# Kernel tuning notes

Measured on AMD Instinct MI355X. Metric: run time of the kernel, lower is better.

The kernel has to match this reference:

```python
import jax, jax.numpy as jnp
import numpy as np

H = 128; F = 64; G = 50; L = 4; CUT = 10.0
M = 256; K = 8; A = 32
N_TOPO = M * A; N = M * K * A; NCONF = M * K
E_CONF = N * 16; E_GRAPH = N_TOPO * 4
ATOM_TYPES = 100; BOND_TYPES = 10
OFFSETS = jnp.linspace(0.0, CUT, G)
GCOEFF = -0.5 / (CUT / (G - 1)) ** 2  # GaussianSmearing coeff
BN_EPS = 1e-5


def batchnorm(x, g, b):
    # BatchNorm1d in training mode: batch statistics over nodes
    mu = x.mean(0)
    var = ((x - mu) ** 2).mean(0)
    return (x - mu) * jax.lax.rsqrt(var + BN_EPS) * g + b


def setup_inputs():
    key = jax.random.key(0)
    ks = jax.random.split(key, 20)
    s = lambda k, shp: (jax.random.normal(k, shp) * 0.05).astype(jnp.float32)
    inp = {}
    inp["x_topo"] = jax.random.randint(ks[0], (N_TOPO,), 0, ATOM_TYPES)
    inp["pos"] = jax.random.normal(ks[1], (N, 3), dtype=jnp.float32) * 3.0
    inp["edge_index_conf"] = jax.random.randint(ks[2], (2, E_CONF), 0, N)
    inp["edge_index_graph"] = jax.random.randint(ks[3], (2, E_GRAPH), 0, N_TOPO)
    inp["edge_attr_graph"] = jax.random.randint(ks[4], (E_GRAPH,), 0, BOND_TYPES)
    # conf_node_batch: for molecule i, repeat arange(A)+i*A over K conformers
    cnb = (np.arange(M)[:, None, None] * A + np.broadcast_to(np.arange(A), (K, A))).reshape(-1)
    inp["conf_node_batch"] = jnp.asarray(cnb, dtype=jnp.int32)
    inp["pos_batch"] = jnp.repeat(jnp.arange(NCONF), A).astype(jnp.int32)
    inp["conf_batch"] = jnp.repeat(jnp.arange(M), K).astype(jnp.int32)
    # parameters
    inp["atom_emb"] = s(ks[5], (ATOM_TYPES, H))
    inp["cf_lin1_w"] = s(ks[6], (L, H, F))
    inp["cf_mlp_w1"] = s(ks[7], (L, G, F)); inp["cf_mlp_b1"] = jnp.zeros((L, F), jnp.float32)
    inp["cf_mlp_w2"] = s(ks[8], (L, F, F)); inp["cf_mlp_b2"] = jnp.zeros((L, F), jnp.float32)
    inp["cf_lin2_w"] = s(ks[9], (L, F, H)); inp["cf_lin2_b"] = jnp.zeros((L, H), jnp.float32)
    inp["lin_w"] = s(ks[10], (L, H, H)); inp["lin_b"] = jnp.zeros((L, H), jnp.float32)
    inp["bond_emb"] = s(ks[11], (L, BOND_TYPES, H))
    inp["gin_w1"] = s(ks[12], (L, H, H)); inp["gin_b1"] = jnp.zeros((L, H), jnp.float32)
    inp["gin_w2"] = s(ks[13], (L, H, H)); inp["gin_b2"] = jnp.zeros((L, H), jnp.float32)
    inp["gin_bn_g"] = jnp.ones((L, H), jnp.float32); inp["gin_bn_b"] = jnp.zeros((L, H), jnp.float32)
    inp["bn_g"] = jnp.ones((L, H), jnp.float32); inp["bn_b"] = jnp.zeros((L, H), jnp.float32)
    inp["gin_eps"] = jnp.zeros((L,), jnp.float32)
    inp["out_w1"] = s(ks[14], (H, H)); inp["out_b1"] = jnp.zeros((H,), jnp.float32)
    inp["out_w2"] = s(ks[15], (H, 1)); inp["out_b2"] = jnp.zeros((1,), jnp.float32)
    return inp


def _forward(x_topo, edge_index_conf, edge_index_graph, edge_attr_graph,
             conf_node_batch, pos_batch, conf_batch,
             pos, atom_emb, cf_lin1_w, cf_mlp_w1, cf_mlp_b1, cf_mlp_w2, cf_mlp_b2,
             cf_lin2_w, cf_lin2_b, lin_w, lin_b, bond_emb,
             gin_w1, gin_b1, gin_w2, gin_b2, gin_bn_g, gin_bn_b, bn_g, bn_b,
             gin_eps, out_w1, out_b1, out_w2, out_b2):
    # AtomEncoder on topo graph, broadcast to all conformers
    x = atom_emb[x_topo][conf_node_batch]                      # [N, H]
    row, col = edge_index_conf[0], edge_index_conf[1]
    d = pos[row] - pos[col]
    ew = jnp.sqrt(jnp.sum(d * d, axis=-1) + 1e-12)             # edge_weight_conf [E_conf]
    ea = jnp.exp(GCOEFF * (ew[:, None] - OFFSETS) ** 2)        # GaussianSmearing [E_conf, G]
    cwin = 0.5 * (jnp.cos(ew * jnp.pi / CUT) + 1.0)            # SchNet cosine cutoff
    gr, gc = edge_index_graph[0], edge_index_graph[1]
    for l in range(L):
        # CFConv branch (use_conf)
        Wf = (jax.nn.relu(ea @ cf_mlp_w1[l] + cf_mlp_b1[l]) @ cf_mlp_w2[l] + cf_mlp_b2[l]) * cwin[:, None]
        h = x @ cf_lin1_w[l]                                   # lin1, no bias
        agg = jax.ops.segment_sum(h[row] * Wf, col, num_segments=N)
        h = agg @ cf_lin2_w[l] + cf_lin2_b[l]                  # lin2
        h = jax.nn.relu(h)
        h = h @ lin_w[l] + lin_b[l]
        out = x + h                                            # residual
        # GIN branch on topo graph (use_graph)
        x_agg = jax.ops.segment_max(x, conf_node_batch, num_segments=N_TOPO)
        eemb = bond_emb[l][edge_attr_graph]                    # BondEncoder
        magg = jax.ops.segment_sum(jax.nn.relu(x_agg[gr] + eemb), gc, num_segments=N_TOPO)
        hg = (1.0 + gin_eps[l]) * x_agg + magg
        hg = jax.nn.relu(batchnorm(hg @ gin_w1[l] + gin_b1[l], gin_bn_g[l], gin_bn_b[l]))
        hg = hg @ gin_w2[l] + gin_b2[l]
        hg = batchnorm(hg, bn_g[l], bn_b[l])
        out = out + hg[conf_node_batch]
        x = jax.nn.relu(out)
    x = jax.ops.segment_max(x, pos_batch, num_segments=NCONF)  # pool atoms -> conformers
    x = jax.ops.segment_max(x, conf_batch, num_segments=M)     # pool conformers -> molecules
    x = jax.nn.relu(x @ out_w1 + out_b1) @ out_w2 + out_b2     # out_layer
    return x                                                   # training mode: no clamp


def reference(x_topo, pos, edge_index_conf, edge_index_graph, edge_attr_graph,
              conf_node_batch, pos_batch, conf_batch,
              atom_emb, cf_lin1_w, cf_mlp_w1, cf_mlp_b1, cf_mlp_w2, cf_mlp_b2,
              cf_lin2_w, cf_lin2_b, lin_w, lin_b, bond_emb,
              gin_w1, gin_b1, gin_w2, gin_b2, gin_bn_g, gin_bn_b, bn_g, bn_b,
              gin_eps, out_w1, out_b1, out_w2, out_b2):
    return _forward(x_topo, edge_index_conf, edge_index_graph, edge_attr_graph,
                    conf_node_batch, pos_batch, conf_batch,
                    pos, atom_emb, cf_lin1_w, cf_mlp_w1, cf_mlp_b1, cf_mlp_w2, cf_mlp_b2,
                    cf_lin2_w, cf_lin2_b, lin_w, lin_b, bond_emb,
                    gin_w1, gin_b1, gin_w2, gin_b2, gin_bn_g, gin_bn_b, bn_g, bn_b,
                    gin_eps, out_w1, out_b1, out_w2, out_b2)
```

## Files before the change

### kernel.cpp

```cpp
#include <hip/hip_runtime.h>
#include <hip/hip_bf16.h>

#define EC 1048576
#define NN 65536
#define NT 8192
#define MM 256
#define HH 128
#define FF 64
#define GG 50
#define EG 32768

#define TBL 2048
#define TBL_SHIFT 11
#define TRANGE 14.0f

#define CAP 32
#define OVF_CAP 8192
#define GCAP 32
#define GOVF_CAP 1024
#define NEB (NN * 64 / 256)

#define SENT 0xFFE00000

constexpr float STEP = 10.0f / 49.0f;
constexpr float GC = -0.5f / (STEP * STEP);

typedef __attribute__((ext_vector_type(8))) short bf16x8;
typedef __attribute__((ext_vector_type(4))) float f32x4;

__device__ __forceinline__ ushort f2b(float v) {
    __hip_bfloat16 h = __float2bfloat16(v);
    return *(ushort*)&h;
}
__device__ __forceinline__ float b2f(ushort u) {
    return __uint_as_float(((unsigned)u) << 16);
}

__device__ __forceinline__ void prep_one(
    const float* __restrict__ W, ushort* __restrict__ Wf, int K, int N, int idx)
{
    int sz = K * N;
    int l = idx / sz;
    int t = idx - l * sz;
    int j = t & 7;
    int lane = (t >> 3) & 63;
    int rest = t >> 9;
    int KTl = K >> 5;
    int kt = rest % KTl;
    int nt = rest / KTl;
    int k = kt * 32 + (lane >> 4) * 8 + j;
    int n = nt * 16 + (lane & 15);
    Wf[idx] = f2b(W[(size_t)l * sz + (size_t)k * N + n]);
}

#define SETUP_B0 (EC / 256)
#define SETUP_B1 (SETUP_B0 + EG / 256)
#define SETUP_B2 (SETUP_B1 + NN * HH / 8 / 256)
#define SETUP_B3 (SETUP_B2 + 4 * TBL / 4)
#define SETUP_B4 (SETUP_B3 + 1024)
__global__ __launch_bounds__(256) void setup_kernel(
    const int* __restrict__ eic, const int* __restrict__ cnb,
    const int* __restrict__ eig, const int* __restrict__ eattr,
    const float* __restrict__ pos,
    const float* __restrict__ emb, const int* __restrict__ xtopo,
    ushort* __restrict__ xb,
    int* __restrict__ cntA, int* __restrict__ pay_pad,
    int* __restrict__ ovf_cnt, int2* __restrict__ ovf,
    int* __restrict__ gcnt, int2* __restrict__ gpay_pad, int4* __restrict__ govf,
    const float* __restrict__ mw1, const float* __restrict__ mb1,
    const float* __restrict__ mw2, const float* __restrict__ mb2,
    float* __restrict__ table_all,
    const float* __restrict__ cf_lin1_w, const float* __restrict__ cf_lin2_w,
    const float* __restrict__ lin_w, const float* __restrict__ gin_w1,
    const float* __restrict__ gin_w2,
    ushort* __restrict__ w1f, ushort* __restrict__ w2f, ushort* __restrict__ wlf,
    ushort* __restrict__ gw1f, ushort* __restrict__ gw2f)
{
    int b = blockIdx.x, tid = threadIdx.x;
    if (b < SETUP_B0) {
        int e = b * 256 + tid;
        int r = eic[e], c = eic[EC + e];
        float dx = pos[r*3+0] - pos[c*3+0];
        float dy = pos[r*3+1] - pos[c*3+1];
        float dz = pos[r*3+2] - pos[c*3+2];
        float w = sqrtf(dx*dx + dy*dy + dz*dz + 1e-12f);
        float u = fminf(w * ((TBL - 1) / TRANGE), 2046.96875f);
        int pay = (((int)(u * 32.0f)) << 16) | (r & 0xFFFF);
        int slot = atomicAdd(&cntA[c], 1);
        if (slot < CAP) {
            pay_pad[c * CAP + slot] = pay;
        } else {
            int o = atomicAdd(&ovf_cnt[0], 1);
            if (o < OVF_CAP) ovf[o] = make_int2(c, pay);
        }
    } else if (b < SETUP_B1) {
        int e = (b - SETUP_B0) * 256 + tid;
        int src = eig[e], dst = eig[EG + e];
        int at = eattr[e];
        int slot = atomicAdd(&gcnt[dst], 1);
        if (slot < GCAP) {
            gpay_pad[dst * GCAP + slot] = make_int2(src, at);
        } else {
            int o = atomicAdd(&ovf_cnt[1], 1);
            if (o < GOVF_CAP) govf[o] = make_int4(dst, src, at, 0);
        }
    } else if (b < SETUP_B2) {
        int idx = (b - SETUP_B1) * 256 + tid;
        int n = idx >> 4;
        int f8 = (idx & 15) << 3;
        const float* e = emb + (size_t)xtopo[cnb[n]] * HH + f8;
        float4 v0 = *(const float4*)e;
        float4 v1 = *(const float4*)(e + 4);
        ushort u[8] = {f2b(v0.x), f2b(v0.y), f2b(v0.z), f2b(v0.w),
                       f2b(v1.x), f2b(v1.y), f2b(v1.z), f2b(v1.w)};
        *(bf16x8*)(xb + ((size_t)idx << 3)) = *(const bf16x8*)u;
    } else if (b < SETUP_B3) {
        int entry = (b - SETUP_B2) * 4 + (tid >> 6);
        int l = entry >> TBL_SHIFT;
        int p = entry & (TBL - 1);
        int lane = tid & 63;
        int wv = tid >> 6;
        const float* w1 = mw1 + (size_t)l * GG * FF;
        const float* b1 = mb1 + (size_t)l * FF;
        const float* w2 = mw2 + (size_t)l * FF * FF;
        const float* b2 = mb2 + (size_t)l * FF;
        float w = p * (TRANGE / (TBL - 1));
        float t = b1[lane];
        for (int g = 0; g < GG; g++) {
            float d = w - g * STEP;
            float ea = __expf(GC * d * d);
            t = fmaf(ea, w1[g * 64 + lane], t);
        }
        __shared__ float ts[4][64];
        ts[wv][lane] = fmaxf(t, 0.f);
        __syncthreads();
        float wf = b2[lane];
        for (int i = 0; i < 64; i++)
            wf = fmaf(ts[wv][i], w2[i * 64 + lane], wf);
        float cw = 0.5f * (__cosf(w * (3.14159265358979323846f / 10.0f)) + 1.0f);
        table_all[((size_t)l * TBL + p) * 64 + lane] = wf * cw;
    } else {
        int pb = b - SETUP_B3;
        if (pb < 128)       prep_one(cf_lin1_w, w1f, HH, FF, pb * 256 + tid);
        else if (pb < 256)  prep_one(cf_lin2_w, w2f, FF, HH, (pb - 128) * 256 + tid);
        else if (pb < 512)  prep_one(lin_w, wlf, HH, HH, (pb - 256) * 256 + tid);
        else if (pb < 768)  prep_one(gin_w1, gw1f, HH, HH, (pb - 512) * 256 + tid);
        else                prep_one(gin_w2, gw2f, HH, HH, (pb - 768) * 256 + tid);
    }
}

#define S2_B0 (4 * TBL * 64 / 256)
#define S2_B1 (S2_B0 + NN / 64)
__global__ __launch_bounds__(256) void stage2_kernel(
    const float* __restrict__ table_all, ushort2* __restrict__ table2_all,
    const ushort* __restrict__ A, const ushort* __restrict__ Bf,
    ushort* __restrict__ Cb)
{
    int b = blockIdx.x, tid = threadIdx.x;
    if (b < S2_B0) {
        int idx = b * 256 + tid;
        int f = idx & 63;
        int rest = idx >> 6;
        int i = rest & (TBL - 1);
        int l = rest >> TBL_SHIFT;
        if (i == TBL - 1) {
            table2_all[idx] = make_ushort2(0, 0);
            return;
        }
        const float* T = table_all + ((size_t)l * TBL) * 64;
        float t0 = T[(size_t)i * 64 + f];
        float t1 = T[(size_t)(i + 1) * 64 + f];
        table2_all[idx] = make_ushort2(f2b(t0), f2b((t1 - t0) * 0.03125f));
    } else {
        int wave = tid >> 6, lane = tid & 63;
        int m0 = ((b - S2_B0) * 4 + wave) * 16;
        int arow = m0 + (lane & 15);
        int ak = (lane >> 4) * 8;
        bf16x8 a[4];
        const ushort* Ap = A + (size_t)arow * 128 + ak;
        #pragma unroll
        for (int kt = 0; kt < 4; kt++)
            a[kt] = *(const bf16x8*)(Ap + kt * 32);
        f32x4 acc[4];
        #pragma unroll
        for (int i = 0; i < 4; i++) acc[i] = (f32x4){0.f, 0.f, 0.f, 0.f};
        const ushort* Bp = Bf + (size_t)lane * 8;
        #pragma unroll
        for (int nt = 0; nt < 4; nt++)
            #pragma unroll
            for (int kt = 0; kt < 4; kt++) {
                bf16x8 bb = *(const bf16x8*)(Bp + ((size_t)(nt * 4 + kt)) * 512);
                acc[nt] = __builtin_amdgcn_mfma_f32_16x16x32_bf16(a[kt], bb, acc[nt], 0, 0, 0);
            }
        int col0 = lane & 15;
        int rbase = m0 + (lane >> 4) * 4;
        #pragma unroll
        for (int nt = 0; nt < 4; nt++) {
            int col = nt * 16 + col0;
            #pragma unroll
            for (int r = 0; r < 4; r++)
                Cb[(size_t)(rbase + r) * 64 + col] = f2b(acc[nt][r]);
        }
    }
}

#define EDGE8(BASE) { \
    int pq[8]; \
    { int4 q0 = *(const int4*)(pp + BASE); \
      int4 q1 = *(const int4*)(pp + BASE + 4); \
      pq[0]=__builtin_amdgcn_readfirstlane(q0.x); \
      pq[1]=__builtin_amdgcn_readfirstlane(q0.y); \
      pq[2]=__builtin_amdgcn_readfirstlane(q0.z); \
      pq[3]=__builtin_amdgcn_readfirstlane(q0.w); \
      pq[4]=__builtin_amdgcn_readfirstlane(q1.x); \
      pq[5]=__builtin_amdgcn_readfirstlane(q1.y); \
      pq[6]=__builtin_amdgcn_readfirstlane(q1.z); \
      pq[7]=__builtin_amdgcn_readfirstlane(q1.w); } \
    float h[8]; \
    _Pragma("unroll") \
    for (int q = 0; q < 8; q++) \
        h[q] = b2f(*(const ushort*)(h1c + ((((unsigned)(pq[q] & 0xFFFF)) << 7) + lane2))); \
    unsigned tt[8]; \
    _Pragma("unroll") \
    for (int q = 0; q < 8; q++) \
        tt[q] = *(const unsigned*)(tbc + (((((unsigned)pq[q]) >> 21) << 8) + lane4)); \
    _Pragma("unroll") \
    for (int q = 0; q < 8; q++) { \
        float fr = (float)((unsigned)((pq[q] >> 16) & 31)); \
        float t0 = __uint_as_float(tt[q] << 16); \
        float dts = __uint_as_float(tt[q] & 0xFFFF0000u); \
        float wf = fmaf(dts, fr, t0); \
        if (q & 1) acc1 = fmaf(h[q], wf, acc1); else acc0 = fmaf(h[q], wf, acc0); \
    } }

#define EDGE4(BASE) { \
    int pq[4]; \
    { int4 q0 = *(const int4*)(pp + BASE); \
      pq[0]=__builtin_amdgcn_readfirstlane(q0.x); \
      pq[1]=__builtin_amdgcn_readfirstlane(q0.y); \
      pq[2]=__builtin_amdgcn_readfirstlane(q0.z); \
      pq[3]=__builtin_amdgcn_readfirstlane(q0.w); } \
    float h[4]; \
    _Pragma("unroll") \
    for (int q = 0; q < 4; q++) \
        h[q] = b2f(*(const ushort*)(h1c + ((((unsigned)(pq[q] & 0xFFFF)) << 7) + lane2))); \
    unsigned tt[4]; \
    _Pragma("unroll") \
    for (int q = 0; q < 4; q++) \
        tt[q] = *(const unsigned*)(tbc + (((((unsigned)pq[q]) >> 21) << 8) + lane4)); \
    _Pragma("unroll") \
    for (int q = 0; q < 4; q++) { \
        float fr = (float)((unsigned)((pq[q] >> 16) & 31)); \
        float t0 = __uint_as_float(tt[q] << 16); \
        float dts = __uint_as_float(tt[q] & 0xFFFF0000u); \
        float wf = fmaf(dts, fr, t0); \
        if (q & 1) acc1 = fmaf(h[q], wf, acc1); else acc0 = fmaf(h[q], wf, acc0); \
    } }

__global__ __launch_bounds__(256) void edge_xagg_kernel(
    const int* __restrict__ cntA, const int* __restrict__ pay_pad,
    const int* __restrict__ ovf_cnt, const int2* __restrict__ ovf,
    const ushort2* __restrict__ table2, const ushort* __restrict__ h1b,
    ushort* __restrict__ aggb,
    const ushort* __restrict__ xb, ushort* __restrict__ xaggb)
{
    int tid = threadIdx.x;
    if (blockIdx.x < NEB) {
        int lane = tid & 63;
        int node = __builtin_amdgcn_readfirstlane((blockIdx.x * 256 + tid) >> 6);
        unsigned lane2 = (unsigned)lane * 2;
        unsigned lane4 = (unsigned)lane * 4;
        const char* h1c = (const char*)h1b;
        const char* tbc = (const char*)table2;
        int deg = cntA[node];
        int n1 = min(deg, CAP);
        const int* pp = pay_pad + (size_t)node * CAP;
        float acc0 = 0.f, acc1 = 0.f;
        EDGE8(0);
        if (n1 > 8) {
            EDGE8(8);
            if (n1 > 16) {
                EDGE4(16);
                if (n1 > 20) {
                    EDGE4(20);
                    if (n1 > 24) {
                        EDGE4(24);
                        if (n1 > 28) EDGE4(28);
                    }
                }
            }
        }
        float acc = acc0 + acc1;
        if (deg > CAP) {
            int no = min(ovf_cnt[0], OVF_CAP);
            for (int j = 0; j < no; j++) {
                int2 o = ovf[j];
                if (o.x == node) {
                    unsigned uf = (unsigned)o.y >> 16;
                    int i0 = uf >> 5;
                    float fr = (float)(uf & 31);
                    ushort2 ttv = table2[(size_t)i0 * 64 + lane];
                    acc = fmaf(b2f(h1b[(size_t)(o.y & 0xFFFF) * 64 + lane]),
                               fmaf(b2f(ttv.y), fr, b2f(ttv.x)), acc);
                }
            }
        }
        aggb[(size_t)node * 64 + lane] = f2b(acc);
    } else {
        int idx = (blockIdx.x - NEB) * 256 + tid;
        int tn = idx >> 7, f = idx & 127;
        int m = tn >> 5, a = tn & 31;
        const ushort* base = xb + ((size_t)((m << 8) + a)) * HH + f;
        float mx = -3.4e38f;
        #pragma unroll
        for (int k = 0; k < 8; k++)
            mx = fmaxf(mx, b2f(base[(size_t)(k << 5) * HH]));
        xaggb[idx] = f2b(mx);
    }
}

#define TSTR 136

__global__ __launch_bounds__(128) void gin_gemm1_kernel(
    const int* __restrict__ gcnt, const int2* __restrict__ gpay_pad,
    const int* __restrict__ ovf_cnt, const int4* __restrict__ govf,
    const ushort* __restrict__ xaggb, const float* __restrict__ bemb,
    const float* __restrict__ eps, const ushort* __restrict__ Bf,
    const float* __restrict__ bias, ushort* __restrict__ Cb,
    float* __restrict__ gsum, float* __restrict__ gsq)
{
    __shared__ ushort hg0s[32 * TSTR];
    __shared__ float ssum[128], ssq[128];
    int tid = threadIdx.x;
    ssum[tid] = 0.f; ssq[tid] = 0.f;
    {
        int row = tid >> 2;
        int fc = (tid & 3) * 32;
        int tn = blockIdx.x * 32 + row;
        float e1 = 1.0f + eps[0];
        float acc[32];
        const ushort* xo = xaggb + (size_t)tn * HH + fc;
        #pragma unroll
        for (int c = 0; c < 4; c++) {
            bf16x8 x = *(const bf16x8*)(xo + c * 8);
            #pragma unroll
            for (int j = 0; j < 8; j++)
                acc[c * 8 + j] = e1 * b2f((ushort)x[j]);
        }
        int deg = gcnt[tn];
        int gn = min(deg, GCAP);
        const int2* gp = gpay_pad + (size_t)tn * GCAP;
        for (int p = 0; p < gn; p++) {
            int2 g = gp[p];
            const ushort* xs = xaggb + (size_t)g.x * HH + fc;
            const float* bs = bemb + (size_t)g.y * HH + fc;
            #pragma unroll
            for (int c = 0; c < 4; c++) {
                bf16x8 x = *(const bf16x8*)(xs + c * 8);
                float4 b0 = *(const float4*)(bs + c * 8);
                float4 b1 = *(const float4*)(bs + c * 8 + 4);
                float bb[8] = {b0.x, b0.y, b0.z, b0.w, b1.x, b1.y, b1.z, b1.w};
                #pragma unroll
                for (int j = 0; j < 8; j++)
                    acc[c * 8 + j] += fmaxf(b2f((ushort)x[j]) + bb[j], 0.f);
            }
        }
        if (deg > GCAP) {
            int no = min(ovf_cnt[1], GOVF_CAP);
            for (int j2 = 0; j2 < no; j2++) {
                int4 o = govf[j2];
                if (o.x == tn) {
                    const ushort* xs = xaggb + (size_t)o.y * HH + fc;
                    const float* bs = bemb + (size_t)o.z * HH + fc;
                    #pragma unroll
                    for (int c = 0; c < 4; c++) {
                        bf16x8 x = *(const bf16x8*)(xs + c * 8);
                        float4 b0 = *(const float4*)(bs + c * 8);
                        float4 b1 = *(const float4*)(bs + c * 8 + 4);
                        float bb[8] = {b0.x, b0.y, b0.z, b0.w, b1.x, b1.y, b1.z, b1.w};
                        #pragma unroll
                        for (int j = 0; j < 8; j++)
                            acc[c * 8 + j] += fmaxf(b2f((ushort)x[j]) + bb[j], 0.f);
                    }
                }
            }
        }
        ushort* dst = hg0s + row * TSTR + fc;
        #pragma unroll
        for (int j = 0; j < 32; j++) dst[j] = f2b(acc[j]);
    }
    __syncthreads();
    int wave = tid >> 6, lane = tid & 63;
    int lm = lane & 15, lq = lane >> 4;
    int ak = lq * 8;
    bf16x8 a[4];
    #pragma unroll
    for (int kt = 0; kt < 4; kt++)
        a[kt] = *(const bf16x8*)&hg0s[(wave * 16 + lm) * TSTR + ak + kt * 32];
    f32x4 acc[8];
    #pragma unroll
    for (int i = 0; i < 8; i++) acc[i] = (f32x4){0.f, 0.f, 0.f, 0.f};
    const ushort* Bp = Bf + (size_t)lane * 8;
    #pragma unroll
    for (int nt = 0; nt < 8; nt++)
        #pragma unroll
        for (int kt = 0; kt < 4; kt++) {
            bf16x8 b = *(const bf16x8*)(Bp + ((size_t)(nt * 4 + kt)) * 512);
            acc[nt] = __builtin_amdgcn_mfma_f32_16x16x32_bf16(a[kt], b, acc[nt], 0, 0, 0);
        }
    int rbase = blockIdx.x * 32 + wave * 16 + lq * 4;
    #pragma unroll
    for (int nt = 0; nt < 8; nt++) {
        int col = nt * 16 + lm;
        float bs = bias[col];
        float ps = 0.f, pq = 0.f;
        #pragma unroll
        for (int r = 0; r < 4; r++) {
            float v = acc[nt][r] + bs;
            Cb[(size_t)(rbase + r) * 128 + col] = f2b(v);
            ps += v; pq += v * v;
        }
        atomicAdd(&ssum[col], ps);
        atomicAdd(&ssq[col], pq);
    }
    __syncthreads();
    atomicAdd(&gsum[tid], ssum[tid]);
    atomicAdd(&gsq[tid], ssq[tid]);
}

__global__ __launch_bounds__(128) void gemm_bn_stats_kernel(
    const ushort* __restrict__ Araw, const float* __restrict__ sum1,
    const float* __restrict__ sq1, const float* __restrict__ g1,
    const float* __restrict__ bb1, const ushort* __restrict__ Bf,
    const float* __restrict__ bias, ushort* __restrict__ Cb,
    float* __restrict__ gsum, float* __restrict__ gsq)
{
    __shared__ float ssum[128], ssq[128];
    int tid = threadIdx.x;
    ssum[tid] = 0.f; ssq[tid] = 0.f;
    __syncthreads();
    int wave = tid >> 6, lane = tid & 63;
    int m0 = (blockIdx.x * 2 + wave) * 16;
    int arow = m0 + (lane & 15);
    int ak = (lane >> 4) * 8;
    const float INV_NT = 1.0f / NT;
    bf16x8 a[4];
    const ushort* Ap = Araw + (size_t)arow * 128 + ak;
    #pragma unroll
    for (int kt = 0; kt < 4; kt++) {
        bf16x8 raw = *(const bf16x8*)(Ap + kt * 32);
        ushort ub[8];
        #pragma unroll
        for (int j = 0; j < 8; j++) {
            int k = ak + kt * 32 + j;
            float mu = sum1[k] * INV_NT;
            float var = sq1[k] * INV_NT - mu * mu;
            float inv = rsqrtf(var + 1e-5f);
            float w = fmaxf((b2f((ushort)raw[j]) - mu) * inv * g1[k] + bb1[k], 0.f);
            ub[j] = f2b(w);
        }
        a[kt] = *(bf16x8*)ub;
    }
    f32x4 acc[8];
    #pragma unroll
    for (int i = 0; i < 8; i++) acc[i] = (f32x4){0.f, 0.f, 0.f, 0.f};
    const ushort* Bp = Bf + (size_t)lane * 8;
    #pragma unroll
    for (int nt = 0; nt < 8; nt++)
        #pragma unroll
        for (int kt = 0; kt < 4; kt++) {
            bf16x8 b = *(const bf16x8*)(Bp + ((size_t)(nt * 4 + kt)) * 512);
            acc[nt] = __builtin_amdgcn_mfma_f32_16x16x32_bf16(a[kt], b, acc[nt], 0, 0, 0);
        }
    int col0 = lane & 15;
    int rbase = m0 + (lane >> 4) * 4;
    #pragma unroll
    for (int nt = 0; nt < 8; nt++) {
        int col = nt * 16 + col0;
        float bs = bias[col];
        float ps = 0.f, pq = 0.f;
        #pragma unroll
        for (int r = 0; r < 4; r++) {
            float v = acc[nt][r] + bs;
            Cb[(size_t)(rbase + r) * 128 + col] = f2b(v);
            ps += v; pq += v * v;
        }
        atomicAdd(&ssum[col], ps);
        atomicAdd(&ssq[col], pq);
    }
    __syncthreads();
    atomicAdd(&gsum[tid], ssum[tid]);
    atomicAdd(&gsq[tid], ssq[tid]);
}

__global__ __launch_bounds__(256) void fused_lin_kernel(
    const ushort* __restrict__ aggb, const ushort* __restrict__ w2,
    const float* __restrict__ b2, const ushort* __restrict__ w3,
    const float* __restrict__ b3, const ushort* __restrict__ hgBb,
    const float* __restrict__ sum2, const float* __restrict__ sq2,
    const float* __restrict__ g2, const float* __restrict__ bb2,
    const int* __restrict__ cnb, const ushort* __restrict__ w1n,
    ushort* __restrict__ xb, ushort* __restrict__ h1b)
{
    __shared__ ushort t1s[4][16 * TSTR];
    __shared__ ushort t2s[4][16 * TSTR];
    int tid = threadIdx.x;
    int wave = tid >> 6, lane = tid & 63;
    int m0 = (blockIdx.x * 4 + wave) * 16;
    int lm = lane & 15;
    int lq = lane >> 4;
    ushort* T1 = t1s[wave];
    ushort* T2 = t2s[wave];
    const float INV_NT = 1.0f / NT;

    const ushort* Ap = aggb + (size_t)(m0 + lm) * 64 + lq * 8;
    bf16x8 a1[2];
    a1[0] = *(const bf16x8*)(Ap);
    a1[1] = *(const bf16x8*)(Ap + 32);
    f32x4 acc[8];
    #pragma unroll
    for (int i = 0; i < 8; i++) acc[i] = (f32x4){0.f, 0.f, 0.f, 0.f};
    {
        const ushort* Bp = w2 + (size_t)lane * 8;
        #pragma unroll
        for (int nt = 0; nt < 8; nt++)
            #pragma unroll
            for (int kt = 0; kt < 2; kt++) {
                bf16x8 b = *(const bf16x8*)(Bp + ((size_t)(nt * 2 + kt)) * 512);
                acc[nt] = __builtin_amdgcn_mfma_f32_16x16x32_bf16(a1[kt], b, acc[nt], 0, 0, 0);
            }
    }
    #pragma unroll
    for (int nt = 0; nt < 8; nt++) {
        int col = nt * 16 + lm;
        float bs = b2[col];
        #pragma unroll
        for (int r = 0; r < 4; r++) {
            float v = fmaxf(acc[nt][r] + bs, 0.f);
            T1[(lq * 4 + r) * TSTR + col] = f2b(v);
        }
    }
    __syncthreads();

    bf16x8 a2[4];
    #pragma unroll
    for (int kt = 0; kt < 4; kt++)
        a2[kt] = *(const bf16x8*)&T1[lm * TSTR + kt * 32 + lq * 8];
    __syncthreads();
    #pragma unroll
    for (int i = 0; i < 4; i++) {
        int idx = i * 64 + lane;
        int row = idx >> 4, ch = idx & 15;
        bf16x8 v = *(const bf16x8*)(xb + (size_t)(m0 + row) * HH + ch * 8);
        *(bf16x8*)&T1[row * TSTR + ch * 8] = v;
    }
    #pragma unroll
    for (int i = 0; i < 8; i++) acc[i] = (f32x4){0.f, 0.f, 0.f, 0.f};
    {
        const ushort* Bp = w3 + (size_t)lane * 8;
        #pragma unroll
        for (int nt = 0; nt < 8; nt++)
            #pragma unroll
            for (int kt = 0; kt < 4; kt++) {
                bf16x8 b = *(const bf16x8*)(Bp + ((size_t)(nt * 4 + kt)) * 512);
                acc[nt] = __builtin_amdgcn_mfma_f32_16x16x32_bf16(a2[kt], b, acc[nt], 0, 0, 0);
            }
    }
    int rbase = m0 + lq * 4;
    int cn[4];
    #pragma unroll
    for (int r = 0; r < 4; r++) cn[r] = cnb[rbase + r];
    #pragma unroll
    for (int nt = 0; nt < 8; nt++) {
        int col = nt * 16 + lm;
        float bs = b3[col];
        float mu2 = sum2[col] * INV_NT;
        float var2 = sq2[col] * INV_NT - mu2 * mu2;
        float sc2 = rsqrtf(var2 + 1e-5f) * g2[col];
        float sh2 = bb2[col] - mu2 * sc2;
        #pragma unroll
        for (int r = 0; r < 4; r++) {
            float v = acc[nt][r] + bs;
            v += b2f(T1[(lq * 4 + r) * TSTR + col]);
            v = fmaf(b2f(hgBb[(size_t)cn[r] * HH + col]), sc2, v + sh2);
            v = fmaxf(v, 0.f);
            T2[(lq * 4 + r) * TSTR + col] = f2b(v);
        }
    }
    __syncthreads();
    #pragma unroll
    for (int i = 0; i < 4; i++) {
        int idx = i * 64 + lane;
        int row = idx >> 4, ch = idx & 15;
        bf16x8 v = *(const bf16x8*)&T2[row * TSTR + ch * 8];
        *(bf16x8*)(xb + (size_t)(m0 + row) * HH + ch * 8) = v;
    }
    if (!w1n) return;
    __syncthreads();

    bf16x8 a3[4];
    #pragma unroll
    for (int kt = 0; kt < 4; kt++)
        a3[kt] = *(const bf16x8*)&T2[lm * TSTR + kt * 32 + lq * 8];
    f32x4 acc3[4];
    #pragma unroll
    for (int i = 0; i < 4; i++) acc3[i] = (f32x4){0.f, 0.f, 0.f, 0.f};
    {
        const ushort* Bp = w1n + (size_t)lane * 8;
        #pragma unroll
        for (int nt = 0; nt < 4; nt++)
            #pragma unroll
            for (int kt = 0; kt < 4; kt++) {
                bf16x8 b = *(const bf16x8*)(Bp + ((size_t)(nt * 4 + kt)) * 512);
                acc3[nt] = __builtin_amdgcn_mfma_f32_16x16x32_bf16(a3[kt], b, acc3[nt], 0, 0, 0);
            }
    }
    #pragma unroll
    for (int nt = 0; nt < 4; nt++) {
        int col = nt * 16 + lm;
        #pragma unroll
        for (int r = 0; r < 4; r++)
            T1[(lq * 4 + r) * TSTR + col] = f2b(acc3[nt][r]);
    }
    __syncthreads();
    #pragma unroll
    for (int i = 0; i < 2; i++) {
        int idx = i * 64 + lane;
        int row = idx >> 3, ch = idx & 7;
        bf16x8 v = *(const bf16x8*)&T1[row * TSTR + ch * 8];
        *(bf16x8*)(h1b + (size_t)(m0 + row) * FF + ch * 8) = v;
    }
}

__global__ __launch_bounds__(128) void out_layer_kernel(
    const ushort* __restrict__ xb, const float* __restrict__ w1,
    const float* __restrict__ b1, const float* __restrict__ w2,
    const float* __restrict__ b2, float* __restrict__ out)
{
    int m = blockIdx.x, f = threadIdx.x;
    const ushort* base = xb + (size_t)m * 256 * HH + f;
    float mx = -3.4e38f;
    for (int r = 0; r < 256; r++)
        mx = fmaxf(mx, b2f(base[(size_t)r * HH]));
    __shared__ float xs[128];
    xs[f] = mx;
    __syncthreads();
    float acc = b1[f];
    for (int k = 0; k < 128; k++) acc = fmaf(xs[k], w1[k * HH + f], acc);
    acc = fmaxf(acc, 0.f) * w2[f];
    __shared__ float red[128];
    red[f] = acc;
    __syncthreads();
    for (int off = 64; off > 0; off >>= 1) {
        if (f < off) red[f] += red[f + off];
        __syncthreads();
    }
    if (f == 0) out[m] = red[0] + b2[0];
}

extern "C" void kernel_launch(void* const* d_in, const int* in_sizes, int n_in,
                              void* d_out, int out_size, void* d_ws, size_t ws_size,
                              hipStream_t stream)
{
    const int*   x_topo    = (const int*)d_in[0];
    const float* pos       = (const float*)d_in[1];
    const int*   eic       = (const int*)d_in[2];
    const int*   eig       = (const int*)d_in[3];
    const int*   eattr     = (const int*)d_in[4];
    const int*   cnb       = (const int*)d_in[5];
    const float* atom_emb  = (const float*)d_in[8];
    const float* cf_lin1_w = (const float*)d_in[9];
    const float* cf_mlp_w1 = (const float*)d_in[10];
    const float* cf_mlp_b1 = (const float*)d_in[11];
    const float* cf_mlp_w2 = (const float*)d_in[12];
    const float* cf_mlp_b2 = (const float*)d_in[13];
    const float* cf_lin2_w = (const float*)d_in[14];
    const float* cf_lin2_b = (const float*)d_in[15];
    const float* lin_w     = (const float*)d_in[16];
    const float* lin_b     = (const float*)d_in[17];
    const float* bond_emb  = (const float*)d_in[18];
    const float* gin_w1    = (const float*)d_in[19];
    const float* gin_b1    = (const float*)d_in[20];
    const float* gin_w2    = (const float*)d_in[21];
    const float* gin_b2    = (const float*)d_in[22];
    const float* gin_bn_g  = (const float*)d_in[23];
    const float* gin_bn_b  = (const float*)d_in[24];
    const float* bn_g      = (const float*)d_in[25];
    const float* bn_b      = (const float*)d_in[26];
    const float* gin_eps   = (const float*)d_in[27];
    const float* out_w1    = (const float*)d_in[28];
    const float* out_b1    = (const float*)d_in[29];
    const float* out_w2    = (const float*)d_in[30];
    const float* out_b2    = (const float*)d_in[31];
    float* out = (float*)d_out;

    char* wsb = (char*)d_ws;
    size_t off = 0;
    auto alloc = [&](size_t nbytes) -> void* {
        void* p = (void*)(wsb + off);
        off += (nbytes + 255) & ~(size_t)255;
        return p;
    };
    ushort* xb      = (ushort*)alloc((size_t)NN * HH * 2);
    ushort* h1b     = (ushort*)alloc((size_t)NN * FF * 2);
    ushort* aggb    = (ushort*)alloc((size_t)NN * FF * 2);
    ushort* xaggb   = (ushort*)alloc((size_t)NT * HH * 2);
    ushort* hgA     = (ushort*)alloc((size_t)NT * HH * 2);
    ushort* hgB     = (ushort*)alloc((size_t)NT * HH * 2);
    float*  table_all  = (float*)alloc((size_t)4 * TBL * 64 * 4);
    ushort2* table2_all = (ushort2*)alloc((size_t)4 * TBL * 64 * 4);
    float*  stats   = (float*)alloc((size_t)4 * 4 * 128 * 4);
    int*    cntA    = (int*)alloc((size_t)NN * 4);
    int*    gcnt    = (int*)alloc((size_t)NT * 4);
    int*    ovf_cnt = (int*)alloc(256);
    int*    pay_pad = (int*)alloc((size_t)NN * CAP * 4);
    int2*   ovf     = (int2*)alloc((size_t)OVF_CAP * 8);
    int2*   gpay_pad = (int2*)alloc((size_t)NT * GCAP * 8);
    int4*   govf    = (int4*)alloc((size_t)GOVF_CAP * 16);
    ushort* w1f     = (ushort*)alloc((size_t)4 * HH * FF * 2);
    ushort* w2f     = (ushort*)alloc((size_t)4 * FF * HH * 2);
    ushort* wlf     = (ushort*)alloc((size_t)4 * HH * HH * 2);
    ushort* gw1f    = (ushort*)alloc((size_t)4 * HH * HH * 2);
    ushort* gw2f    = (ushort*)alloc((size_t)4 * HH * HH * 2);

    hipMemsetAsync(stats, 0,
        ((size_t)4 * 4 * 128 * 4 + 255 & ~(size_t)255) +
        ((size_t)NN * 4 + 255 & ~(size_t)255) +
        ((size_t)NT * 4 + 255 & ~(size_t)255) + 256, stream);
    hipMemsetD32Async((hipDeviceptr_t)pay_pad, SENT, (size_t)NN * CAP, stream);

    setup_kernel<<<SETUP_B4, 256, 0, stream>>>(
        eic, cnb, eig, eattr, pos, atom_emb, x_topo, xb,
        cntA, pay_pad, ovf_cnt, ovf, gcnt, gpay_pad, govf,
        cf_mlp_w1, cf_mlp_b1, cf_mlp_w2, cf_mlp_b2, table_all,
        cf_lin1_w, cf_lin2_w, lin_w, gin_w1, gin_w2, w1f, w2f, wlf, gw1f, gw2f);
    stage2_kernel<<<S2_B1, 256, 0, stream>>>(table_all, table2_all, xb, w1f, h1b);

    for (int l = 0; l < 4; l++) {
        const ushort2* table2 = table2_all + (size_t)l * TBL * 64;
        float* sum1 = stats + (size_t)l * 512;
        float* sq1  = sum1 + 128;
        float* sum2 = sum1 + 256;
        float* sq2  = sum1 + 384;
        edge_xagg_kernel<<<NEB + NT * HH / 256, 256, 0, stream>>>(
            cntA, pay_pad, ovf_cnt, ovf, table2, h1b, aggb, xb, xaggb);
        gin_gemm1_kernel<<<NT / 32, 128, 0, stream>>>(
            gcnt, gpay_pad, ovf_cnt, govf, xaggb, bond_emb + (size_t)l * 10 * HH, gin_eps + l,
            gw1f + (size_t)l * HH * HH, gin_b1 + (size_t)l * HH, hgA, sum1, sq1);
        gemm_bn_stats_kernel<<<NT / 32, 128, 0, stream>>>(
            hgA, sum1, sq1, gin_bn_g + (size_t)l * HH, gin_bn_b + (size_t)l * HH,
            gw2f + (size_t)l * HH * HH, gin_b2 + (size_t)l * HH, hgB, sum2, sq2);
        fused_lin_kernel<<<NN / 64, 256, 0, stream>>>(
            aggb, w2f + (size_t)l * FF * HH, cf_lin2_b + (size_t)l * HH,
            wlf + (size_t)l * HH * HH, lin_b + (size_t)l * HH,
            hgB, sum2, sq2, bn_g + (size_t)l * HH, bn_b + (size_t)l * HH,
            cnb, (l < 3) ? (w1f + (size_t)(l + 1) * HH * FF) : nullptr,
            xb, h1b);
    }

    out_layer_kernel<<<MM, 128, 0, stream>>>(xb, out_w1, out_b1, out_w2, out_b2, out);
}
```

Baseline: 584.7 us.

## Fuse GIN aggregation GEMM into edge kernel; vectorize and relocate conformer max-pool

```diff
diff --git a/kernel.cpp b/kernel.cpp
--- a/kernel.cpp
+++ b/kernel.cpp
@@ -149,12 +149,36 @@
     }
 }
 
+__device__ __forceinline__ void xagg_unit(
+    int idx, const ushort* __restrict__ xb, ushort* __restrict__ xaggb)
+{
+    int tn = idx >> 4;
+    int f8 = (idx & 15) << 3;
+    int m = tn >> 5, a = tn & 31;
+    const ushort* base = xb + ((size_t)((m << 8) + a)) * HH + f8;
+    float mx[8];
+    #pragma unroll
+    for (int j = 0; j < 8; j++) mx[j] = -3.4e38f;
+    #pragma unroll
+    for (int k = 0; k < 8; k++) {
+        bf16x8 v = *(const bf16x8*)(base + (size_t)(k << 5) * HH);
+        #pragma unroll
+        for (int j = 0; j < 8; j++) mx[j] = fmaxf(mx[j], b2f((ushort)v[j]));
+    }
+    ushort u[8];
+    #pragma unroll
+    for (int j = 0; j < 8; j++) u[j] = f2b(mx[j]);
+    *(bf16x8*)(xaggb + (size_t)tn * HH + f8) = *(const bf16x8*)u;
+}
+
 #define S2_B0 (4 * TBL * 64 / 256)
-#define S2_B1 (S2_B0 + NN / 64)
+#define S2_G  (NN / 64)
+#define S2_X  (NT * HH / 8 / 256)
+#define S2_B1 (S2_B0 + S2_G + S2_X)
 __global__ __launch_bounds__(256) void stage2_kernel(
     const float* __restrict__ table_all, ushort2* __restrict__ table2_all,
     const ushort* __restrict__ A, const ushort* __restrict__ Bf,
-    ushort* __restrict__ Cb)
+    ushort* __restrict__ Cb, ushort* __restrict__ xaggb)
 {
     int b = blockIdx.x, tid = threadIdx.x;
     if (b < S2_B0) {
@@ -171,7 +195,7 @@
         float t0 = T[(size_t)i * 64 + f];
         float t1 = T[(size_t)(i + 1) * 64 + f];
         table2_all[idx] = make_ushort2(f2b(t0), f2b((t1 - t0) * 0.03125f));
-    } else {
+    } else if (b < S2_B0 + S2_G) {
         int wave = tid >> 6, lane = tid & 63;
         int m0 = ((b - S2_B0) * 4 + wave) * 16;
         int arow = m0 + (lane & 15);
@@ -201,7 +225,15 @@
             for (int r = 0; r < 4; r++)
                 Cb[(size_t)(rbase + r) * 64 + col] = f2b(acc[nt][r]);
         }
-    }
+    } else {
+        xagg_unit((b - S2_B0 - S2_G) * 256 + tid, A, xaggb);
+    }
+}
+
+__global__ __launch_bounds__(256) void xagg_kernel(
+    const ushort* __restrict__ xb, ushort* __restrict__ xaggb)
+{
+    xagg_unit(blockIdx.x * 256 + threadIdx.x, xb, xaggb);
 }
 
 #define EDGE8(BASE) { \
@@ -257,13 +289,22 @@
         if (q & 1) acc1 = fmaf(h[q], wf, acc1); else acc0 = fmaf(h[q], wf, acc0); \
     } }
 
-__global__ __launch_bounds__(256) void edge_xagg_kernel(
+#define TSTR 136
+
+__global__ __launch_bounds__(256) void layer_a_kernel(
     const int* __restrict__ cntA, const int* __restrict__ pay_pad,
     const int* __restrict__ ovf_cnt, const int2* __restrict__ ovf,
     const ushort2* __restrict__ table2, const ushort* __restrict__ h1b,
     ushort* __restrict__ aggb,
-    const ushort* __restrict__ xb, ushort* __restrict__ xaggb)
-{
+    const int* __restrict__ gcnt, const int2* __restrict__ gpay_pad,
+    const int4* __restrict__ govf,
+    const ushort* __restrict__ xaggb, const float* __restrict__ bemb,
+    const float* __restrict__ eps, const ushort* __restrict__ Bf,
+    const float* __restrict__ bias, ushort* __restrict__ Cb,
+    float* __restrict__ gsum, float* __restrict__ gsq)
+{
+    __shared__ ushort hg0s[64 * TSTR];
+    __shared__ float ssum[128], ssq[128];
     int tid = threadIdx.x;
     if (blockIdx.x < NEB) {
         int lane = tid & 63;
@@ -307,125 +348,104 @@
         }
         aggb[(size_t)node * 64 + lane] = f2b(acc);
     } else {
-        int idx = (blockIdx.x - NEB) * 256 + tid;
-        int tn = idx >> 7, f = idx & 127;
-        int m = tn >> 5, a = tn & 31;
-        const ushort* base = xb + ((size_t)((m << 8) + a)) * HH + f;
-        float mx = -3.4e38f;
-        #pragma unroll
-        for (int k = 0; k < 8; k++)
-            mx = fmaxf(mx, b2f(base[(size_t)(k << 5) * HH]));
-        xaggb[idx] = f2b(mx);
-    }
-}
-
-#define TSTR 136
-
-__global__ __launch_bounds__(128) void gin_gemm1_kernel(
-    const int* __restrict__ gcnt, const int2* __restrict__ gpay_pad,
-    const int* __restrict__ ovf_cnt, const int4* __restrict__ govf,
-    const ushort* __restrict__ xaggb, const float* __restrict__ bemb,
-    const float* __restrict__ eps, const ushort* __restrict__ Bf,
-    const float* __restrict__ bias, ushort* __restrict__ Cb,
-    float* __restrict__ gsum, float* __restrict__ gsq)
-{
-    __shared__ ushort hg0s[32 * TSTR];
-    __shared__ float ssum[128], ssq[128];
-    int tid = threadIdx.x;
-    ssum[tid] = 0.f; ssq[tid] = 0.f;
-    {
-        int row = tid >> 2;
-        int fc = (tid & 3) * 32;
-        int tn = blockIdx.x * 32 + row;
-        float e1 = 1.0f + eps[0];
-        float acc[32];
-        const ushort* xo = xaggb + (size_t)tn * HH + fc;
-        #pragma unroll
-        for (int c = 0; c < 4; c++) {
-            bf16x8 x = *(const bf16x8*)(xo + c * 8);
-            #pragma unroll
-            for (int j = 0; j < 8; j++)
-                acc[c * 8 + j] = e1 * b2f((ushort)x[j]);
-        }
-        int deg = gcnt[tn];
-        int gn = min(deg, GCAP);
-        const int2* gp = gpay_pad + (size_t)tn * GCAP;
-        for (int p = 0; p < gn; p++) {
-            int2 g = gp[p];
-            const ushort* xs = xaggb + (size_t)g.x * HH + fc;
-            const float* bs = bemb + (size_t)g.y * HH + fc;
+        int u = blockIdx.x - NEB;
+        if (tid < 128) { ssum[tid] = 0.f; ssq[tid] = 0.f; }
+        {
+            int row = tid >> 2;
+            int fc = (tid & 3) * 32;
+            int tn = u * 64 + row;
+            float e1 = 1.0f + eps[0];
+            float acc[32];
+            const ushort* xo = xaggb + (size_t)tn * HH + fc;
             #pragma unroll
             for (int c = 0; c < 4; c++) {
-                bf16x8 x = *(const bf16x8*)(xs + c * 8);
-                float4 b0 = *(const float4*)(bs + c * 8);
-                float4 b1 = *(const float4*)(bs + c * 8 + 4);
-                float bb[8] = {b0.x, b0.y, b0.z, b0.w, b1.x, b1.y, b1.z, b1.w};
+                bf16x8 x = *(const bf16x8*)(xo + c * 8);
                 #pragma unroll
                 for (int j = 0; j < 8; j++)
-                    acc[c * 8 + j] += fmaxf(b2f((ushort)x[j]) + bb[j], 0.f);
-            }
-        }
-        if (deg > GCAP) {
-            int no = min(ovf_cnt[1], GOVF_CAP);
-            for (int j2 = 0; j2 < no; j2++) {
-                int4 o = govf[j2];
-                if (o.x == tn) {
-                    const ushort* xs = xaggb + (size_t)o.y * HH + fc;
-                    const float* bs = bemb + (size_t)o.z * HH + fc;
+                    acc[c * 8 + j] = e1 * b2f((ushort)x[j]);
+            }
+            int deg = gcnt[tn];
+            int gn = min(deg, GCAP);
+            const int2* gp = gpay_pad + (size_t)tn * GCAP;
+            for (int p = 0; p < gn; p++) {
+                int2 g = gp[p];
+                const ushort* xs = xaggb + (size_t)g.x * HH + fc;
+                const float* bs = bemb + (size_t)g.y * HH + fc;
+                #pragma unroll
+                for (int c = 0; c < 4; c++) {
+                    bf16x8 x = *(const bf16x8*)(xs + c * 8);
+                    float4 b0 = *(const float4*)(bs + c * 8);
+                    float4 b1 = *(const float4*)(bs + c * 8 + 4);
+                    float bb[8] = {b0.x, b0.y, b0.z, b0.w, b1.x, b1.y, b1.z, b1.w};
                     #pragma unroll
-                    for (int c = 0; c < 4; c++) {
-                        bf16x8 x = *(const bf16x8*)(xs + c * 8);
-                        float4 b0 = *(const float4*)(bs + c * 8);
-                        float4 b1 = *(const float4*)(bs + c * 8 + 4);
-                        float bb[8] = {b0.x, b0.y, b0.z, b0.w, b1.x, b1.y, b1.z, b1.w};
+                    for (int j = 0; j < 8; j++)
+                        acc[c * 8 + j] += fmaxf(b2f((ushort)x[j]) + bb[j], 0.f);
+                }
+            }
+            if (deg > GCAP) {
+                int no = min(ovf_cnt[1], GOVF_CAP);
+                for (int j2 = 0; j2 < no; j2++) {
+                    int4 o = govf[j2];
+                    if (o.x == tn) {
+                        const ushort* xs = xaggb + (size_t)o.y * HH + fc;
+                        const float* bs = bemb + (size_t)o.z * HH + fc;
                         #pragma unroll
-                        for (int j = 0; j < 8; j++)
-                            acc[c * 8 + j] += fmaxf(b2f((ushort)x[j]) + bb[j], 0.f);
+                        for (int c = 0; c < 4; c++) {
+                            bf16x8 x = *(const bf16x8*)(xs + c * 8);
+                            float4 b0 = *(const float4*)(bs + c * 8);
+                            float4 b1 = *(const float4*)(bs + c * 8 + 4);
+                            float bb[8] = {b0.x, b0.y, b0.z, b0.w, b1.x, b1.y, b1.z, b1.w};
+                            #pragma unroll
+                            for (int j = 0; j < 8; j++)
+                                acc[c * 8 + j] += fmaxf(b2f((ushort)x[j]) + bb[j], 0.f);
+                        }
                     }
                 }
             }
-        }
-        ushort* dst = hg0s + row * TSTR + fc;
-        #pragma unroll
-        for (int j = 0; j < 32; j++) dst[j] = f2b(acc[j]);
-    }
-    __syncthreads();
-    int wave = tid >> 6, lane = tid & 63;
-    int lm = lane & 15, lq = lane >> 4;
-    int ak = lq * 8;
-    bf16x8 a[4];
-    #pragma unroll
-    for (int kt = 0; kt < 4; kt++)
-        a[kt] = *(const bf16x8*)&hg0s[(wave * 16 + lm) * TSTR + ak + kt * 32];
-    f32x4 acc[8];
-    #pragma unroll
-    for (int i = 0; i < 8; i++) acc[i] = (f32x4){0.f, 0.f, 0.f, 0.f};
-    const ushort* Bp = Bf + (size_t)lane * 8;
-    #pragma unroll
-    for (int nt = 0; nt < 8; nt++)
-        #pragma unroll
-        for (int kt = 0; kt < 4; kt++) {
-            bf16x8 b = *(const bf16x8*)(Bp + ((size_t)(nt * 4 + kt)) * 512);
-            acc[nt] = __builtin_amdgcn_mfma_f32_16x16x32_bf16(a[kt], b, acc[nt], 0, 0, 0);
-        }
-    int rbase = blockIdx.x * 32 + wave * 16 + lq * 4;
-    #pragma unroll
-    for (int nt = 0; nt < 8; nt++) {
-        int col = nt * 16 + lm;
-        float bs = bias[col];
-        float ps = 0.f, pq = 0.f;
-        #pragma unroll
-        for (int r = 0; r < 4; r++) {
-            float v = acc[nt][r] + bs;
-            Cb[(size_t)(rbase + r) * 128 + col] = f2b(v);
-            ps += v; pq += v * v;
-        }
-        atomicAdd(&ssum[col], ps);
-        atomicAdd(&ssq[col], pq);
-    }
-    __syncthreads();
-    atomicAdd(&gsum[tid], ssum[tid]);
-    atomicAdd(&gsq[tid], ssq[tid]);
+            ushort* dst = hg0s + row * TSTR + fc;
+            #pragma unroll
+            for (int j = 0; j < 32; j++) dst[j] = f2b(acc[j]);
+        }
+        __syncthreads();
+        int wave = tid >> 6, lane = tid & 63;
+        int lm = lane & 15, lq = lane >> 4;
+        int ak = lq * 8;
+        bf16x8 a[4];
+        #pragma unroll
+        for (int kt = 0; kt < 4; kt++)
+            a[kt] = *(const bf16x8*)&hg0s[(wave * 16 + lm) * TSTR + ak + kt * 32];
+        f32x4 acc[8];
+        #pragma unroll
+        for (int i = 0; i < 8; i++) acc[i] = (f32x4){0.f, 0.f, 0.f, 0.f};
+        const ushort* Bp = Bf + (size_t)lane * 8;
+        #pragma unroll
+        for (int nt = 0; nt < 8; nt++)
+            #pragma unroll
+            for (int kt = 0; kt < 4; kt++) {
+                bf16x8 b = *(const bf16x8*)(Bp + ((size_t)(nt * 4 + kt)) * 512);
+                acc[nt] = __builtin_amdgcn_mfma_f32_16x16x32_bf16(a[kt], b, acc[nt], 0, 0, 0);
+            }
+        int rbase = u * 64 + wave * 16 + lq * 4;
+        #pragma unroll
+        for (int nt = 0; nt < 8; nt++) {
+            int col = nt * 16 + lm;
+            float bs = bias[col];
+            float ps = 0.f, pq = 0.f;
+            #pragma unroll
+            for (int r = 0; r < 4; r++) {
+                float v = acc[nt][r] + bs;
+                Cb[(size_t)(rbase + r) * 128 + col] = f2b(v);
+                ps += v; pq += v * v;
+            }
+            atomicAdd(&ssum[col], ps);
+            atomicAdd(&ssq[col], pq);
+        }
+        __syncthreads();
+        if (tid < 128) {
+            atomicAdd(&gsum[tid], ssum[tid]);
+            atomicAdd(&gsq[tid], ssq[tid]);
+        }
+    }
 }
 
 __global__ __launch_bounds__(128) void gemm_bn_stats_kernel(
@@ -734,7 +754,7 @@
         cntA, pay_pad, ovf_cnt, ovf, gcnt, gpay_pad, govf,
         cf_mlp_w1, cf_mlp_b1, cf_mlp_w2, cf_mlp_b2, table_all,
         cf_lin1_w, cf_lin2_w, lin_w, gin_w1, gin_w2, w1f, w2f, wlf, gw1f, gw2f);
-    stage2_kernel<<<S2_B1, 256, 0, stream>>>(table_all, table2_all, xb, w1f, h1b);
+    stage2_kernel<<<S2_B1, 256, 0, stream>>>(table_all, table2_all, xb, w1f, h1b, xaggb);
 
     for (int l = 0; l < 4; l++) {
         const ushort2* table2 = table2_all + (size_t)l * TBL * 64;
@@ -742,10 +762,11 @@
         float* sq1  = sum1 + 128;
         float* sum2 = sum1 + 256;
         float* sq2  = sum1 + 384;
-        edge_xagg_kernel<<<NEB + NT * HH / 256, 256, 0, stream>>>(
-            cntA, pay_pad, ovf_cnt, ovf, table2, h1b, aggb, xb, xaggb);
-        gin_gemm1_kernel<<<NT / 32, 128, 0, stream>>>(
-            gcnt, gpay_pad, ovf_cnt, govf, xaggb, bond_emb + (size_t)l * 10 * HH, gin_eps + l,
+        if (l > 0)
+            xagg_kernel<<<NT * HH / 8 / 256, 256, 0, stream>>>(xb, xaggb);
+        layer_a_kernel<<<NEB + NT / 64, 256, 0, stream>>>(
+            cntA, pay_pad, ovf_cnt, ovf, table2, h1b, aggb,
+            gcnt, gpay_pad, govf, xaggb, bond_emb + (size_t)l * 10 * HH, gin_eps + l,
             gw1f + (size_t)l * HH * HH, gin_b1 + (size_t)l * HH, hgA, sum1, sq1);
         gemm_bn_stats_kernel<<<NT / 32, 128, 0, stream>>>(
             hgA, sum1, sq1, gin_bn_g + (size_t)l * HH, gin_bn_b + (size_t)l * HH,
```

Measured after the change: 728.7 us. 24.6% more time.
